# Kernel optimization log

Measured on AMD Instinct MI355X. Metric: run time of the kernel, lower is better.

The kernel has to match this reference:

```python
import jax, jax.numpy as jnp
import numpy as np
from jax import lax
jax.config.update("jax_enable_x64", True)

FNV_OFF = np.int64(-3750763034362895579)
FNV_PRIME = np.int64(4294967731)
I64_MAX = np.iinfo(np.int64).max
INF = np.float32(1e38)
CHUNK = 512  # cluster-chunk size for the cdist fallback


def _pack_key(b, c, vx, vy, vz):
    # five-word FNV-1a 64-bit hash with natural int64 wraparound
    h = jnp.full(b.shape, FNV_OFF, dtype=jnp.int64)
    for w in (b, c, vx, vy, vz):
        h = (h ^ w.astype(jnp.int64)) * FNV_PRIME
    return h


def _safe_norm(x):
    s = jnp.sum(x * x, axis=1)
    n = jnp.sqrt(jnp.where(s > 0, s, 1.0))
    return jnp.where(s > 0, n, 0.0)


def setup_inputs() -> dict:
    key = jax.random.key(0)
    k1, k2, k3, k4 = jax.random.split(key, 4)
    N = 65536
    grid = jax.random.randint(k1, (N, 3), 0, 400).astype(jnp.float32)
    batch_id = jnp.sort(jax.random.randint(k2, (N,), 0, 2).astype(jnp.int64))
    label = jax.random.randint(k3, (N,), 0, 8).astype(jnp.int64)
    pred_off = jax.random.normal(k4, (N, 3), dtype=jnp.float32)
    return {"pred_off": pred_off, "grid": grid, "label": label, "batch_id": batch_id,
            "base_grid": 16, "num_cls": 8, "num_batch": 2}


def _forward(pred_off, grid, label, batch_id, base_grid, num_cls, num_batch):
    N = grid.shape[0]
    grid_f = grid.astype(jnp.float32)
    vox = jnp.floor(grid_f / base_grid).astype(jnp.int64)  # [N,3]

    # voxel_grid: bucket by (batch, voxel) -> consecutive cluster ids via unique
    ckey = ((batch_id * 1024 + vox[:, 0]) * 1024 + vox[:, 1]) * 1024 + vox[:, 2]
    _, cluster = jnp.unique(ckey, return_inverse=True, size=N, fill_value=I64_MAX)
    cluster = cluster.reshape(-1)

    # cluster stats (segment scatter-reduce, num_segments = N upper bound)
    cnt = jax.ops.segment_sum(jnp.ones((N,), jnp.float32), cluster, num_segments=N)
    cl_center = jax.ops.segment_sum(grid_f, cluster, num_segments=N) / jnp.maximum(cnt, 1.0)[:, None]
    cl_batch = jax.ops.segment_min(batch_id, cluster, num_segments=N)
    cl_lbl_lo = jax.ops.segment_min(label, cluster, num_segments=N)
    cl_lbl_hi = jax.ops.segment_max(label, cluster, num_segments=N)
    cl_vox = jax.ops.segment_min(vox, cluster, num_segments=N)
    valid_cl = cnt > 0
    pure_cl = (cl_lbl_lo == cl_lbl_hi) & valid_cl
    pure_pt = pure_cl[cluster]

    # hash table of pure clusters, sorted by key (invalid -> sentinel, sorts last)
    pk_all = jnp.where(pure_cl, _pack_key(cl_batch, cl_lbl_lo, cl_vox[:, 0], cl_vox[:, 1], cl_vox[:, 2]), I64_MAX)
    order = jnp.argsort(pk_all)
    pk_sort = pk_all[order]
    pc_sort = cl_center[order]
    ok_sort = pure_cl[order]

    # per (batch,label) global centers
    key_bl = batch_id * num_cls + label
    nbl = num_batch * num_cls
    cnt_bl = jax.ops.segment_sum(jnp.ones((N,), jnp.float32), key_bl, num_segments=nbl)
    global_c = jax.ops.segment_sum(grid_f, key_bl, num_segments=nbl) / jnp.maximum(cnt_bl, 1.0)[:, None]
    step_sign = jnp.sign(global_c[key_bl] - cl_center[cluster]).astype(jnp.int64)  # [N,3]

    # +/-1 and +/-2 voxel hash lookup (steps 1 and K+1=2)
    def probe(step):
        cv = cl_vox[cluster] + step_sign * step
        ck = _pack_key(batch_id, label, cv[:, 0], cv[:, 1], cv[:, 2])
        idx = jnp.searchsorted(pk_sort, ck)
        idxc = jnp.minimum(idx, N - 1)
        hit = (idx < N) & ok_sort[idxc] & (pk_sort[idxc] == ck)
        return hit, pc_sort[idxc]

    hit1, t1 = probe(1)
    hit2, t2 = probe(2)
    hit_pt = hit1 | hit2
    tgt_c = jnp.where(hit1[:, None], t1, jnp.where(hit2[:, None], t2, grid_f))

    # fallback: nearest pure-cluster center with same (batch,label), chunked cdist+argmin
    miss = (~pure_pt) & (~hit_pt)
    code_y = key_bl
    code_x = jnp.where(pure_cl, cl_batch * num_cls + cl_lbl_lo, jnp.int64(-1))
    p2 = jnp.sum(grid_f * grid_f, axis=1)  # [N]

    def body(carry, i):
        best_d, best_c = carry
        c = lax.dynamic_slice_in_dim(cl_center, i * CHUNK, CHUNK)   # [S,3]
        cc = lax.dynamic_slice_in_dim(code_x, i * CHUNK, CHUNK)      # [S]
        d2 = p2[:, None] - 2.0 * (grid_f @ c.T) + jnp.sum(c * c, axis=1)[None, :]  # [N,S]
        d2 = jnp.where(cc[None, :] == code_y[:, None], d2, INF)
        j = jnp.argmin(d2, axis=1)
        dmin = jnp.take_along_axis(d2, j[:, None], axis=1)[:, 0]
        upd = dmin < best_d
        best_d = jnp.where(upd, dmin, best_d)
        best_c = jnp.where(upd[:, None], c[j], best_c)
        return (best_d, best_c), None

    nchunk = N // CHUNK
    (best_d, best_c), _ = lax.scan(body, (jnp.full((N,), INF, jnp.float32), grid_f), jnp.arange(nchunk))
    tgt_c = jnp.where((miss & (best_d < INF))[:, None], best_c, tgt_c)

    # loss: smooth-L1 on offsets below 99th-percentile magnitude + direction cosine loss
    tgt_off = tgt_c - grid_f
    mag = _safe_norm(tgt_off)
    thresh = jnp.quantile(mag, 0.99)
    m1 = mag <= thresh
    d = pred_off - tgt_off
    ad = jnp.abs(d)
    hub = jnp.where(ad < 1.0, 0.5 * d * d, ad - 0.5)
    n1 = jnp.sum(m1).astype(jnp.float32)
    loss_l1 = jnp.where(n1 > 0, jnp.sum(hub * m1[:, None]) / jnp.maximum(n1 * 3.0, 1.0), 0.0)

    md = (mag > 0) & m1
    eps = 1e-4
    pn = _safe_norm(pred_off)
    cos = jnp.sum(pred_off * tgt_off, axis=1) / jnp.maximum(pn * mag, eps)
    nmd = jnp.sum(md).astype(jnp.float32)
    loss_dir = jnp.where(nmd > 0, 1.0 - jnp.sum(cos * md) / jnp.maximum(nmd, 1.0), 0.0)
    return jnp.stack([loss_l1.astype(jnp.float32), loss_dir.astype(jnp.float32)])


def reference(pred_off, grid, label, batch_id, base_grid, num_cls, num_batch):
    return _forward(pred_off, grid, label, batch_id, base_grid, num_cls, num_batch)
```

## Files before the change

### kernel.cpp

```cpp
#include <hip/hip_runtime.h>
#include <climits>

#define VOXD 25
#define SLOT3 (VOXD*VOXD*VOXD)
#define SLOTS (2*SLOT3)
#define NCLS 8
#define NCODE 16
#define NBLK ((SLOTS + 255) / 256)
#define HB 2048
#define BPC 64
#define TILE 1024
#define CSTRIDE SLOT3

struct Scalars {
  double hub;
  double cosSum;
  int n1;
  int nmd;
  float thresh;
  int done;
  int done2;
};

__device__ __forceinline__ int voxslot(int b, int vx, int vy, int vz) {
  return ((b * VOXD + vx) * VOXD + vy) * VOXD + vz;
}

__device__ __forceinline__ int block_scan256(int v, int* ws) {
  int lane = threadIdx.x & 63, w = threadIdx.x >> 6;
  int s = v;
  #pragma unroll
  for (int off = 1; off < 64; off <<= 1) {
    int t = __shfl_up(s, off, 64);
    if (lane >= off) s += t;
  }
  if (lane == 63) ws[w] = s;
  __syncthreads();
  int add = 0;
  #pragma unroll
  for (int q = 0; q < 4; ++q) if (q < w) add += ws[q];
  __syncthreads();
  return s + add;
}

__global__ void k_scatter(const float* __restrict__ grid, const int* __restrict__ label,
                          const int* __restrict__ batch,
                          unsigned long long* vA, unsigned long long* vB, int* lmask,
                          int* blCnt, float* blSum, int n) {
  __shared__ int sCnt[NCODE];
  __shared__ float sSum[3 * NCODE];
  int tid = threadIdx.x;
  if (tid < NCODE) sCnt[tid] = 0;
  if (tid < 3 * NCODE) sSum[tid] = 0.f;
  __syncthreads();
  int i = blockIdx.x * blockDim.x + tid;
  if (i < n) {
    float gx = grid[3*i], gy = grid[3*i+1], gz = grid[3*i+2];
    int ix = (int)gx, iy = (int)gy, iz = (int)gz;
    int vx = (int)floorf(gx * (1.0f/16.0f));
    int vy = (int)floorf(gy * (1.0f/16.0f));
    int vz = (int)floorf(gz * (1.0f/16.0f));
    int b = batch[i], l = label[i];
    int s = voxslot(b, vx, vy, vz);
    atomicAdd(&vA[s], ((unsigned long long)(unsigned)ix << 32) | (unsigned)iy);
    atomicAdd(&vB[s], ((unsigned long long)(unsigned)iz << 24) | 1ULL);
    atomicOr(&lmask[s], 1 << l);
    int bl = b * NCLS + l;
    atomicAdd(&sCnt[bl], 1);
    atomicAdd(&sSum[3*bl], gx); atomicAdd(&sSum[3*bl+1], gy); atomicAdd(&sSum[3*bl+2], gz);
  }
  __syncthreads();
  if (tid < NCODE && sCnt[tid] != 0) atomicAdd(&blCnt[tid], sCnt[tid]);
  if (tid < 3 * NCODE && sSum[tid] != 0.f) atomicAdd(&blSum[tid], sSum[tid]);
}

__global__ void k_prep(const unsigned long long* vA, const unsigned long long* vB,
                       const int* lmask, float4* ctr, float4* pC, int* codeCnt) {
  __shared__ int lc[NCODE];
  __shared__ int lb[NCODE];
  int tid = threadIdx.x;
  if (tid < NCODE) lc[tid] = 0;
  __syncthreads();
  int s = blockIdx.x * 256 + tid;
  int code = -1, lpos = 0;
  float4 v = make_float4(0.f, 0.f, 0.f, __int_as_float(-2));
  if (s < SLOTS) {
    unsigned long long bq = vB[s];
    unsigned c = (unsigned)(bq & 0xFFFFFFULL);
    if (c > 0) {
      unsigned long long aq = vA[s];
      float fc = (float)c;
      float cx = __fdiv_rn((float)(unsigned)(aq >> 32), fc);
      float cy = __fdiv_rn((float)(unsigned)(aq & 0xFFFFFFFFULL), fc);
      float cz = __fdiv_rn((float)(unsigned)(bq >> 24), fc);
      int m = lmask[s];
      bool pure = (m & (m - 1)) == 0;
      int lbl = __ffs(m) - 1;
      v = make_float4(cx, cy, cz, __int_as_float(pure ? lbl : -1));
      if (pure) {
        code = (s / SLOT3) * NCLS + lbl;
        lpos = atomicAdd(&lc[code], 1);
      }
    }
    ctr[s] = v;
  }
  __syncthreads();
  if (tid < NCODE) lb[tid] = (lc[tid] > 0) ? atomicAdd(&codeCnt[tid], lc[tid]) : 0;
  __syncthreads();
  if (code >= 0) {
    int pos = code * CSTRIDE + lb[code] + lpos;
    pC[pos] = make_float4(v.x, v.y, v.z, __int_as_float(s));
  }
}

__global__ void k_targets(const float* __restrict__ grid, const int* __restrict__ label,
                          const int* __restrict__ batch,
                          const float4* __restrict__ ctr,
                          const int* __restrict__ blCnt, const float* __restrict__ blSum,
                          float* tgt, float* mag, int* ghist,
                          int* missPart, int* missCnt, int mstride, int n) {
  __shared__ int wCnt[4][NCODE];
  __shared__ int gBase[NCODE];
  __shared__ int h[HB];
  int tid = threadIdx.x, lane = tid & 63, w = tid >> 6;
  for (int t = tid; t < HB; t += 256) h[t] = 0;
  __syncthreads();
  int i = blockIdx.x * blockDim.x + tid;
  bool active = (i < n);
  bool miss = false;
  int mcode = -1;

  if (active) {
    float gx = grid[3*i], gy = grid[3*i+1], gz = grid[3*i+2];
    int vx = (int)floorf(gx * (1.0f/16.0f));
    int vy = (int)floorf(gy * (1.0f/16.0f));
    int vz = (int)floorf(gz * (1.0f/16.0f));
    int b = batch[i], l = label[i];
    int s = voxslot(b, vx, vy, vz);

    float4 own = ctr[s];
    bool purept = (__float_as_int(own.w) >= 0);

    int bl = b * NCLS + l;
    float fbc = (float)max(blCnt[bl], 1);
    float gcx = __fdiv_rn(blSum[3*bl],   fbc);
    float gcy = __fdiv_rn(blSum[3*bl+1], fbc);
    float gcz = __fdiv_rn(blSum[3*bl+2], fbc);

    float dx = __fsub_rn(gcx, own.x);
    float dy = __fsub_rn(gcy, own.y);
    float dz = __fsub_rn(gcz, own.z);
    int sgx = (dx > 0.f) ? 1 : ((dx < 0.f) ? -1 : 0);
    int sgy = (dy > 0.f) ? 1 : ((dy < 0.f) ? -1 : 0);
    int sgz = (dz > 0.f) ? 1 : ((dz < 0.f) ? -1 : 0);

    int ax1 = vx + sgx,     ay1 = vy + sgy,     az1 = vz + sgz;
    int ax2 = vx + 2 * sgx, ay2 = vy + 2 * sgy, az2 = vz + 2 * sgz;
    bool v1 = (unsigned)ax1 < (unsigned)VOXD && (unsigned)ay1 < (unsigned)VOXD &&
              (unsigned)az1 < (unsigned)VOXD;
    bool v2 = (unsigned)ax2 < (unsigned)VOXD && (unsigned)ay2 < (unsigned)VOXD &&
              (unsigned)az2 < (unsigned)VOXD;

    float4 q1 = make_float4(0.f, 0.f, 0.f, __int_as_float(-3));
    float4 q2 = q1;
    if (v1) q1 = ctr[voxslot(b, ax1, ay1, az1)];
    if (v2) q2 = ctr[voxslot(b, ax2, ay2, az2)];

    bool hit1 = v1 && (__float_as_int(q1.w) == l);
    bool hit2 = v2 && (__float_as_int(q2.w) == l);
    bool hit = hit1 || hit2;

    float tx = hit1 ? q1.x : (hit2 ? q2.x : gx);
    float ty = hit1 ? q1.y : (hit2 ? q2.y : gy);
    float tz = hit1 ? q1.z : (hit2 ? q2.z : gz);

    tgt[3*i] = tx; tgt[3*i+1] = ty; tgt[3*i+2] = tz;
    miss = (!purept && !hit);
    if (miss) {
      mcode = bl;
    } else {
      float tox = __fsub_rn(tx, gx), toy = __fsub_rn(ty, gy), toz = __fsub_rn(tz, gz);
      float ssq = __fadd_rn(__fadd_rn(__fmul_rn(tox,tox), __fmul_rn(toy,toy)),
                            __fmul_rn(toz,toz));
      float m = (ssq > 0.f) ? sqrtf(ssq) : 0.f;
      mag[i] = m;
      atomicAdd(&h[__float_as_uint(m) >> 21], 1);
    }
  }
  int myrank = 0;
  #pragma unroll
  for (int c = 0; c < NCODE; ++c) {
    unsigned long long mb = __ballot(mcode == c);
    if (lane == 0) wCnt[w][c] = __popcll(mb);
    if (mcode == c) myrank = __popcll(mb & ((1ULL << lane) - 1ULL));
  }
  __syncthreads();
  if (tid < NCODE) {
    int tot = wCnt[0][tid] + wCnt[1][tid] + wCnt[2][tid] + wCnt[3][tid];
    gBase[tid] = (tot > 0) ? atomicAdd(&missCnt[tid], tot) : 0;
  }
  __syncthreads();
  if (miss) {
    int base = gBase[mcode];
    for (int q = 0; q < 4; ++q) if (q < w) base += wCnt[q][mcode];
    missPart[mcode * mstride + base + myrank] = i;
  }
  for (int t = tid; t < HB; t += 256) {
    int c = h[t];
    if (c != 0) atomicAdd(&ghist[t], c);
  }
}

__global__ void __launch_bounds__(256) k_fallback(
    const float* __restrict__ grid,
    const float4* __restrict__ pC,
    const float4* __restrict__ ctr,
    const int* __restrict__ codeCnt,
    const int* __restrict__ missPart, const int* __restrict__ missCnt,
    float* tgt, float* mag, int* ghist, int mstride) {
  __shared__ float4 tile4[TILE];
  __shared__ int    stile[TILE];
  __shared__ unsigned long long bkeyw[4][64];
  __shared__ int h[HB];
  int tid = threadIdx.x, lane = tid & 63, w = tid >> 6;
  int c = blockIdx.x / BPC;
  int y = blockIdx.x % BPC;
  int mc = missCnt[c];
  if (y * 64 >= mc) return;
  int cc = codeCnt[c];
  int j0 = c * CSTRIDE;
  const int* mlist = missPart + c * mstride;

  for (int t = tid; t < HB; t += 256) h[t] = 0;
  __syncthreads();

  for (int t0 = y * 64; t0 < mc; t0 += BPC * 64) {
    int t = t0 + lane;
    bool valid = (t < mc);
    int idx = 0;
    float gx = 0.f, gy = 0.f, gz = 0.f, p2 = 0.f;
    if (valid) {
      idx = mlist[t];
      gx = grid[3*idx]; gy = grid[3*idx+1]; gz = grid[3*idx+2];
      p2 = __fadd_rn(__fadd_rn(__fmul_rn(gx,gx), __fmul_rn(gy,gy)),
                     __fmul_rn(gz,gz));
    }
    unsigned long long key = 0xFFFFFFFFFFFFFFFFULL;
    for (int tb = 0; tb < cc; tb += TILE) {
      int m = min(TILE, cc - tb);
      __syncthreads();
      for (int j = tid; j < m; j += 256) {
        float4 cl = pC[j0 + tb + j];
        float c2 = __fadd_rn(__fadd_rn(__fmul_rn(cl.x,cl.x), __fmul_rn(cl.y,cl.y)),
                             __fmul_rn(cl.z,cl.z));
        tile4[j] = make_float4(cl.x, cl.y, cl.z, c2);
        stile[j] = __float_as_int(cl.w);
      }
      __syncthreads();
      #pragma unroll 4
      for (int j = w; j < m; j += 4) {
        float4 cl = tile4[j];
        float dot = __fadd_rn(__fadd_rn(__fmul_rn(gx,cl.x), __fmul_rn(gy,cl.y)),
                              __fmul_rn(gz,cl.z));
        float d2 = __fadd_rn(__fsub_rn(p2, __fmul_rn(2.0f, dot)), cl.w);
        unsigned fb = __float_as_uint(d2);
        fb = (fb >> 31) ? ~fb : (fb | 0x80000000u);
        unsigned long long k2 = ((unsigned long long)fb << 32) | (unsigned)stile[j];
        if (k2 < key) key = k2;
      }
    }
    bkeyw[w][lane] = key;
    __syncthreads();
    if (w == 0 && valid) {
      unsigned long long k0 = bkeyw[0][lane];
      unsigned long long k1 = bkeyw[1][lane];
      unsigned long long k2_ = bkeyw[2][lane];
      unsigned long long k3 = bkeyw[3][lane];
      unsigned long long kk = k0 < k1 ? k0 : k1;
      unsigned long long kh = k2_ < k3 ? k2_ : k3;
      if (kh < kk) kk = kh;
      float mv = 0.f;
      if (cc > 0) {
        int slot = (int)(unsigned)(kk & 0xFFFFFFFFULL);
        float4 cl = ctr[slot];
        tgt[3*idx] = cl.x; tgt[3*idx+1] = cl.y; tgt[3*idx+2] = cl.z;
        float tox = __fsub_rn(cl.x, gx), toy = __fsub_rn(cl.y, gy),
              toz = __fsub_rn(cl.z, gz);
        float ssq = __fadd_rn(__fadd_rn(__fmul_rn(tox,tox), __fmul_rn(toy,toy)),
                              __fmul_rn(toz,toz));
        mv = (ssq > 0.f) ? sqrtf(ssq) : 0.f;
      }
      mag[idx] = mv;
      atomicAdd(&h[__float_as_uint(mv) >> 21], 1);
    }
    __syncthreads();
  }

  for (int t = tid; t < HB; t += 256) {
    int cv = h[t];
    if (cv != 0) atomicAdd(&ghist[t], cv);
  }
}

__global__ void __launch_bounds__(256) k_loss_sel(
    const float* __restrict__ pred, const float* __restrict__ grid,
    const float* __restrict__ tgt, const float* __restrict__ mag,
    const int* __restrict__ ghist, int* gh2A, int* gh2B,
    unsigned* dBits, double2* dHC, int* uCnt,
    Scalars* sc, float* out, int n, int nblocks, int r0, int r1, double tfrac) {
  __shared__ int h[HB];
  __shared__ int h2[HB];
  __shared__ int ws[4];
  __shared__ int s_misc[8];
  __shared__ double shH[256];
  __shared__ double shC[256];
  __shared__ int shN[256];
  __shared__ int shM[256];
  __shared__ int sLast;
  __shared__ float sTh;
  int tid = threadIdx.x, lane = tid & 63;

  int base8 = tid * 8;
  {
    int cbin[8];
    int s = 0;
    #pragma unroll
    for (int k = 0; k < 8; ++k) { cbin[k] = ghist[base8 + k]; s += cbin[k]; }
    int incl = block_scan256(s, ws);
    int lo = incl - s;
    if (r0 >= lo && r0 < lo + s) {
      int acc = lo;
      #pragma unroll
      for (int k = 0; k < 8; ++k) {
        if (r0 < acc + cbin[k]) { s_misc[0] = base8 + k; s_misc[1] = r0 - acc; break; }
        acc += cbin[k];
      }
    }
    if (r1 >= lo && r1 < lo + s) {
      int acc = lo;
      #pragma unroll
      for (int k = 0; k < 8; ++k) {
        if (r1 < acc + cbin[k]) { s_misc[2] = base8 + k; s_misc[3] = r1 - acc; break; }
        acc += cbin[k];
      }
    }
  }
  __syncthreads();
  int binA = s_misc[0], rA = s_misc[1], binB = s_misc[2], rB = s_misc[3];

  for (int t = tid; t < HB; t += 256) { h[t] = 0; h2[t] = 0; }
  __syncthreads();

  int i = blockIdx.x * 256 + tid;
  double hub = 0.0, cs = 0.0;
  int c1 = 0, cmd = 0;
  bool dfr = false;
  unsigned bits = 0;
  double dhub = 0.0, dcs = 0.0;
  if (i < n) {
    float m = mag[i];
    bits = __float_as_uint(m);
    int cb = (int)(bits >> 21);
    bool boundary = (cb == binA || cb == binB);
    if (boundary || cb < binA) {
      float tox = __fsub_rn(tgt[3*i],   grid[3*i]);
      float toy = __fsub_rn(tgt[3*i+1], grid[3*i+1]);
      float toz = __fsub_rn(tgt[3*i+2], grid[3*i+2]);
      float px = pred[3*i], py = pred[3*i+1], pz = pred[3*i+2];
      float d0 = __fsub_rn(px, tox), d1 = __fsub_rn(py, toy), d2 = __fsub_rn(pz, toz);
      float a0 = fabsf(d0), a1 = fabsf(d1), a2 = fabsf(d2);
      float h0 = (a0 < 1.f) ? __fmul_rn(__fmul_rn(0.5f, d0), d0) : __fsub_rn(a0, 0.5f);
      float h1 = (a1 < 1.f) ? __fmul_rn(__fmul_rn(0.5f, d1), d1) : __fsub_rn(a1, 0.5f);
      float h2v = (a2 < 1.f) ? __fmul_rn(__fmul_rn(0.5f, d2), d2) : __fsub_rn(a2, 0.5f);
      double hubv = (double)h0 + (double)h1 + (double)h2v;
      double csv = 0.0;
      if (m > 0.f) {
        float ps = __fadd_rn(__fadd_rn(__fmul_rn(px,px), __fmul_rn(py,py)), __fmul_rn(pz,pz));
        float pn = (ps > 0.f) ? sqrtf(ps) : 0.f;
        float dotp = __fadd_rn(__fadd_rn(__fmul_rn(px,tox), __fmul_rn(py,toy)),
                               __fmul_rn(pz,toz));
        float den = fmaxf(__fmul_rn(pn, m), 1e-4f);
        csv = (double)__fdiv_rn(dotp, den);
      }
      if (boundary) {
        dfr = true;
        dhub = hubv; dcs = csv;
        if (cb == binA) atomicAdd(&h[(bits >> 10) & 0x7FF], 1);
        if (cb == binB) atomicAdd(&h2[(bits >> 10) & 0x7FF], 1);
      } else {
        c1 = 1;
        hub = hubv;
        if (m > 0.f) { cmd = 1; cs = csv; }
      }
    }
  }
  {
    unsigned long long mb = __ballot(dfr);
    int mcp = __popcll(mb);
    int bs = 0;
    if (lane == 0 && mcp > 0) bs = atomicAdd(uCnt, mcp);
    bs = __shfl(bs, 0, 64);
    if (dfr) {
      int pos = bs + __popcll(mb & ((1ULL << lane) - 1ULL));
      dBits[pos] = bits;
      dHC[pos] = make_double2(dhub, dcs);
    }
  }
  __syncthreads();
  for (int t = tid; t < HB; t += 256) {
    int a = h[t];
    if (a != 0) atomicAdd(&gh2A[t], a);
    int b = h2[t];
    if (b != 0) atomicAdd(&gh2B[t], b);
  }

  shH[tid] = hub; shC[tid] = cs; shN[tid] = c1; shM[tid] = cmd;
  __syncthreads();
  for (int off = 128; off > 0; off >>= 1) {
    if (tid < off) {
      shH[tid] += shH[tid+off];
      shC[tid] += shC[tid+off];
      shN[tid] += shN[tid+off];
      shM[tid] += shM[tid+off];
    }
    __syncthreads();
  }
  if (tid == 0) {
    atomicAdd(&sc->hub, shH[0]);
    atomicAdd(&sc->cosSum, shC[0]);
    atomicAdd(&sc->n1, shN[0]);
    atomicAdd(&sc->nmd, shM[0]);
    __threadfence();
    int d = atomicAdd(&sc->done2, 1);
    sLast = (d == nblocks - 1) ? 1 : 0;
  }
  __syncthreads();
  if (!sLast) return;
  __threadfence();

  int U = atomicAdd(uCnt, 0);

  {
    int a8[8], sA = 0;
    #pragma unroll
    for (int k = 0; k < 8; ++k) { a8[k] = gh2A[base8 + k]; sA += a8[k]; }
    int inclA = block_scan256(sA, ws);
    int accA = inclA - sA;
    #pragma unroll
    for (int k = 0; k < 8; ++k) {
      if (rA >= accA && rA < accA + a8[k]) { s_misc[4] = base8 + k; s_misc[5] = rA - accA; }
      accA += a8[k];
    }
    int b8[8], sB = 0;
    #pragma unroll
    for (int k = 0; k < 8; ++k) { b8[k] = gh2B[base8 + k]; sB += b8[k]; }
    int inclB = block_scan256(sB, ws);
    int accB = inclB - sB;
    #pragma unroll
    for (int k = 0; k < 8; ++k) {
      if (rB >= accB && rB < accB + b8[k]) { s_misc[6] = base8 + k; s_misc[7] = rB - accB; }
      accB += b8[k];
    }
  }
  __syncthreads();
  int subA = s_misc[4], subRA = s_misc[5], subB = s_misc[6], subRB = s_misc[7];

  for (int t = tid; t < 1024; t += 256) { h[t] = 0; h2[t] = 0; }
  __syncthreads();
  {
    const uint4* b4 = (const uint4*)dBits;
    int nv = U >> 2;
    for (int v = tid; v < nv; v += 256) {
      uint4 u = b4[v];
      unsigned bb[4] = { u.x, u.y, u.z, u.w };
      #pragma unroll
      for (int k = 0; k < 4; ++k) {
        unsigned b0 = bb[k];
        int cb = (int)(b0 >> 21);
        if (cb == binA && (int)((b0 >> 10) & 0x7FF) == subA) atomicAdd(&h[b0 & 0x3FF], 1);
        if (cb == binB && (int)((b0 >> 10) & 0x7FF) == subB) atomicAdd(&h2[b0 & 0x3FF], 1);
      }
    }
    for (int t = (nv << 2) + tid; t < U; t += 256) {
      unsigned b0 = dBits[t];
      int cb = (int)(b0 >> 21);
      if (cb == binA && (int)((b0 >> 10) & 0x7FF) == subA) atomicAdd(&h[b0 & 0x3FF], 1);
      if (cb == binB && (int)((b0 >> 10) & 0x7FF) == subB) atomicAdd(&h2[b0 & 0x3FF], 1);
    }
  }
  __syncthreads();
  {
    int base4 = tid * 4;
    int la[4], sA = 0;
    #pragma unroll
    for (int k = 0; k < 4; ++k) { la[k] = h[base4 + k]; sA += la[k]; }
    int inclA = block_scan256(sA, ws);
    int accA = inclA - sA;
    #pragma unroll
    for (int k = 0; k < 4; ++k) {
      if (subRA >= accA && subRA < accA + la[k]) s_misc[0] = base4 + k;
      accA += la[k];
    }
    int lb4[4], sB = 0;
    #pragma unroll
    for (int k = 0; k < 4; ++k) { lb4[k] = h2[base4 + k]; sB += lb4[k]; }
    int inclB = block_scan256(sB, ws);
    int accB = inclB - sB;
    #pragma unroll
    for (int k = 0; k < 4; ++k) {
      if (subRB >= accB && subRB < accB + lb4[k]) s_misc[1] = base4 + k;
      accB += lb4[k];
    }
  }
  __syncthreads();
  if (tid == 0) {
    unsigned va = ((unsigned)binA << 21) | ((unsigned)subA << 10) | (unsigned)s_misc[0];
    unsigned vb = ((unsigned)binB << 21) | ((unsigned)subB << 10) | (unsigned)s_misc[1];
    double a = (double)__uint_as_float(va);
    double b = (double)__uint_as_float(vb);
    double th = (tfrac >= 0.5) ? (b - (b - a) * (1.0 - tfrac)) : (a + (b - a) * tfrac);
    sc->thresh = (float)th;
    sTh = (float)th;
  }
  __syncthreads();
  float th = sTh;

  double hub2 = 0.0, cs2 = 0.0;
  int c12 = 0, cmd2 = 0;
  for (int t = tid; t < U; t += 256) {
    unsigned v = dBits[t];
    float m = __uint_as_float(v);
    double2 hc = dHC[t];
    if (m <= th) {
      c12 += 1;
      hub2 += hc.x;
      if (m > 0.f) { cmd2 += 1; cs2 += hc.y; }
    }
  }
  shH[tid] = hub2; shC[tid] = cs2; shN[tid] = c12; shM[tid] = cmd2;
  __syncthreads();
  for (int off = 128; off > 0; off >>= 1) {
    if (tid < off) {
      shH[tid] += shH[tid+off];
      shC[tid] += shC[tid+off];
      shN[tid] += shN[tid+off];
      shM[tid] += shM[tid+off];
    }
    __syncthreads();
  }
  if (tid == 0) {
    double th_hub = atomicAdd(&sc->hub, 0.0) + shH[0];
    double th_cos = atomicAdd(&sc->cosSum, 0.0) + shC[0];
    int n1 = atomicAdd(&sc->n1, 0) + shN[0];
    int nmd = atomicAdd(&sc->nmd, 0) + shM[0];
    double l1 = (n1 > 0) ? th_hub / fmax((double)n1 * 3.0, 1.0) : 0.0;
    double ld = (nmd > 0) ? (1.0 - th_cos / fmax((double)nmd, 1.0)) : 0.0;
    out[0] = (float)l1;
    out[1] = (float)ld;
  }
}

extern "C" void kernel_launch(void* const* d_in, const int* in_sizes, int n_in,
                              void* d_out, int out_size, void* d_ws, size_t ws_size,
                              hipStream_t stream) {
  const float* pred  = (const float*)d_in[0];
  const float* grid  = (const float*)d_in[1];
  const int*   label = (const int*)d_in[2];
  const int*   batch = (const int*)d_in[3];
  int n = in_sizes[2];
  int mstride = n / 4;

  char* p = (char*)d_ws;
  auto take = [&](size_t bytes) -> char* {
    char* r = p;
    p += (bytes + 255) & ~(size_t)255;
    return r;
  };
  char* zbase = p;
  unsigned long long* vA = (unsigned long long*)take((size_t)SLOTS*8);
  unsigned long long* vB = (unsigned long long*)take((size_t)SLOTS*8);
  int*    lmask    = (int*)   take((size_t)SLOTS*4);
  int*    codeCnt  = (int*)   take(NCODE*4);
  int*    missCnt  = (int*)   take(NCODE*4);
  int*    blCnt    = (int*)   take(16*4);
  float*  blSum    = (float*) take(48*4);
  int*    ghist    = (int*)   take((size_t)HB*4);
  int*    gh2A     = (int*)   take((size_t)HB*4);
  int*    gh2B     = (int*)   take((size_t)HB*4);
  int*    uCnt     = (int*)   take(4);
  Scalars* sc      = (Scalars*)take(sizeof(Scalars));
  size_t zbytes = (size_t)(p - zbase);
  float4* ctr      = (float4*)take((size_t)SLOTS*16);
  float4* pC       = (float4*)take((size_t)NCODE*CSTRIDE*16);
  float*  tgt      = (float*) take((size_t)n*3*4);
  float*  mag      = (float*) take((size_t)n*4);
  int*    missPart = (int*)   take((size_t)NCODE*mstride*4);
  unsigned* dBits  = (unsigned*)take((size_t)n*4);
  double2*  dHC    = (double2*) take((size_t)n*16);

  int nb = (n + 255) / 256;
  int nfb = NCODE * BPC;

  double vi = 0.99 * (double)(n - 1);
  int r0 = (int)vi;
  int r1 = r0 + 1; if (r1 > n - 1) r1 = n - 1;
  double tfrac = vi - (double)r0;

  hipMemsetAsync(zbase, 0, zbytes, stream);
  k_scatter<<<nb, 256, 0, stream>>>(grid, label, batch, vA, vB, lmask,
                                    blCnt, blSum, n);
  k_prep<<<NBLK, 256, 0, stream>>>(vA, vB, lmask, ctr, pC, codeCnt);
  k_targets<<<nb, 256, 0, stream>>>(grid, label, batch, ctr, blCnt, blSum,
                                    tgt, mag, ghist, missPart, missCnt, mstride, n);
  k_fallback<<<nfb, 256, 0, stream>>>(grid, pC, ctr, codeCnt,
                                      missPart, missCnt, tgt, mag, ghist, mstride);
  k_loss_sel<<<nb, 256, 0, stream>>>(pred, grid, tgt, mag, ghist, gh2A, gh2B,
                                     dBits, dHC, uCnt, sc, (float*)d_out,
                                     n, nb, r0, r1, tfrac);
}
```

Before: 138.3 us.

## Fuse voxel prep into targets kernel and recompute centers from raw sums

Removes the separate k_prep kernel and the ctr center array. Pure-cluster compaction into pC now happens at the start of the targets kernel. Own and neighbor centers are recomputed on demand from the vA/vB atomic sums and lmask, and the fallback kernel does the same for its winning cluster. Part of the workspace zeroing moves from the memset into k_scatter, shrinking the memset to the accumulator arrays. This saves one launch and the ctr write/read traffic, at the cost of extra divisions and more scattered loads per point.

```diff
diff --git a/kernel.cpp b/kernel.cpp
--- a/kernel.cpp
+++ b/kernel.cpp
@@ -6,7 +6,6 @@
 #define SLOTS (2*SLOT3)
 #define NCLS 8
 #define NCODE 16
-#define NBLK ((SLOTS + 255) / 256)
 #define HB 2048
 #define BPC 64
 #define TILE 1024
@@ -46,10 +45,15 @@
 __global__ void k_scatter(const float* __restrict__ grid, const int* __restrict__ label,
                           const int* __restrict__ batch,
                           unsigned long long* vA, unsigned long long* vB, int* lmask,
-                          int* blCnt, float* blSum, int n) {
+                          int* blCnt, float* blSum, int* lateZero, int nzi, int n) {
   __shared__ int sCnt[NCODE];
   __shared__ float sSum[3 * NCODE];
   int tid = threadIdx.x;
+  {
+    int g = blockIdx.x * 256 + tid;
+    int stride = gridDim.x * 256;
+    for (int t = g; t < nzi; t += stride) lateZero[t] = 0;
+  }
   if (tid < NCODE) sCnt[tid] = 0;
   if (tid < 3 * NCODE) sSum[tid] = 0.f;
   __syncthreads();
@@ -74,63 +78,59 @@
   if (tid < 3 * NCODE && sSum[tid] != 0.f) atomicAdd(&blSum[tid], sSum[tid]);
 }
 
-__global__ void k_prep(const unsigned long long* vA, const unsigned long long* vB,
-                       const int* lmask, float4* ctr, float4* pC, int* codeCnt) {
-  __shared__ int lc[NCODE];
-  __shared__ int lb[NCODE];
-  int tid = threadIdx.x;
-  if (tid < NCODE) lc[tid] = 0;
-  __syncthreads();
-  int s = blockIdx.x * 256 + tid;
-  int code = -1, lpos = 0;
-  float4 v = make_float4(0.f, 0.f, 0.f, __int_as_float(-2));
-  if (s < SLOTS) {
-    unsigned long long bq = vB[s];
-    unsigned c = (unsigned)(bq & 0xFFFFFFULL);
-    if (c > 0) {
-      unsigned long long aq = vA[s];
-      float fc = (float)c;
-      float cx = __fdiv_rn((float)(unsigned)(aq >> 32), fc);
-      float cy = __fdiv_rn((float)(unsigned)(aq & 0xFFFFFFFFULL), fc);
-      float cz = __fdiv_rn((float)(unsigned)(bq >> 24), fc);
-      int m = lmask[s];
-      bool pure = (m & (m - 1)) == 0;
-      int lbl = __ffs(m) - 1;
-      v = make_float4(cx, cy, cz, __int_as_float(pure ? lbl : -1));
-      if (pure) {
-        code = (s / SLOT3) * NCLS + lbl;
-        lpos = atomicAdd(&lc[code], 1);
-      }
-    }
-    ctr[s] = v;
-  }
-  __syncthreads();
-  if (tid < NCODE) lb[tid] = (lc[tid] > 0) ? atomicAdd(&codeCnt[tid], lc[tid]) : 0;
-  __syncthreads();
-  if (code >= 0) {
-    int pos = code * CSTRIDE + lb[code] + lpos;
-    pC[pos] = make_float4(v.x, v.y, v.z, __int_as_float(s));
-  }
-}
-
-__global__ void k_targets(const float* __restrict__ grid, const int* __restrict__ label,
-                          const int* __restrict__ batch,
-                          const float4* __restrict__ ctr,
-                          const int* __restrict__ blCnt, const float* __restrict__ blSum,
-                          float* tgt, float* mag, int* ghist,
-                          int* missPart, int* missCnt, int mstride, int n) {
+__global__ void __launch_bounds__(256) k_targets_prep(
+    const float* __restrict__ grid, const int* __restrict__ label,
+    const int* __restrict__ batch,
+    const unsigned long long* __restrict__ vA, const unsigned long long* __restrict__ vB,
+    const int* __restrict__ lmask,
+    const int* __restrict__ blCnt, const float* __restrict__ blSum,
+    float4* pC, int* codeCnt,
+    float* tgt, float* mag, int* ghist,
+    int* missPart, int* missCnt, int mstride, int spb, int n) {
   __shared__ int wCnt[4][NCODE];
   __shared__ int gBase[NCODE];
   __shared__ int h[HB];
+  __shared__ int lc[NCODE];
+  __shared__ int lb[NCODE];
   int tid = threadIdx.x, lane = tid & 63, w = tid >> 6;
   for (int t = tid; t < HB; t += 256) h[t] = 0;
-  __syncthreads();
+  if (tid < NCODE) lc[tid] = 0;
+  __syncthreads();
+
+  int code = -1, lpos = 0;
+  int sSlot = blockIdx.x * spb + tid;
+  float pcx = 0.f, pcy = 0.f, pcz = 0.f;
+  if (tid < spb && sSlot < SLOTS) {
+    unsigned long long bq = vB[sSlot];
+    unsigned c = (unsigned)(bq & 0xFFFFFFULL);
+    if (c > 0) {
+      unsigned long long aq = vA[sSlot];
+      float fc = (float)c;
+      pcx = __fdiv_rn((float)(unsigned)(aq >> 32), fc);
+      pcy = __fdiv_rn((float)(unsigned)(aq & 0xFFFFFFFFULL), fc);
+      pcz = __fdiv_rn((float)(unsigned)(bq >> 24), fc);
+      int m = lmask[sSlot];
+      bool pure = (m & (m - 1)) == 0;
+      if (pure) {
+        int lbl = __ffs(m) - 1;
+        code = (sSlot / SLOT3) * NCLS + lbl;
+        lpos = atomicAdd(&lc[code], 1);
+      }
+    }
+  }
+  __syncthreads();
+  if (tid < NCODE) lb[tid] = (lc[tid] > 0) ? atomicAdd(&codeCnt[tid], lc[tid]) : 0;
+  __syncthreads();
+  if (code >= 0) {
+    int pos = code * CSTRIDE + lb[code] + lpos;
+    pC[pos] = make_float4(pcx, pcy, pcz, __int_as_float(sSlot));
+  }
+
   int i = blockIdx.x * blockDim.x + tid;
-  bool active = (i < n);
   bool miss = false;
   int mcode = -1;
 
-  if (active) {
+  if (i < n) {
     float gx = grid[3*i], gy = grid[3*i+1], gz = grid[3*i+2];
     int vx = (int)floorf(gx * (1.0f/16.0f));
     int vy = (int)floorf(gy * (1.0f/16.0f));
@@ -138,8 +138,15 @@
     int b = batch[i], l = label[i];
     int s = voxslot(b, vx, vy, vz);
 
-    float4 own = ctr[s];
-    bool purept = (__float_as_int(own.w) >= 0);
+    unsigned long long bqo = vB[s];
+    unsigned co = (unsigned)(bqo & 0xFFFFFFULL);
+    unsigned long long aqo = vA[s];
+    float fco = (float)co;
+    float ownx = __fdiv_rn((float)(unsigned)(aqo >> 32), fco);
+    float owny = __fdiv_rn((float)(unsigned)(aqo & 0xFFFFFFFFULL), fco);
+    float ownz = __fdiv_rn((float)(unsigned)(bqo >> 24), fco);
+    int mo = lmask[s];
+    bool purept = (mo & (mo - 1)) == 0;
 
     int bl = b * NCLS + l;
     float fbc = (float)max(blCnt[bl], 1);
@@ -147,9 +154,9 @@
     float gcy = __fdiv_rn(blSum[3*bl+1], fbc);
     float gcz = __fdiv_rn(blSum[3*bl+2], fbc);
 
-    float dx = __fsub_rn(gcx, own.x);
-    float dy = __fsub_rn(gcy, own.y);
-    float dz = __fsub_rn(gcz, own.z);
+    float dx = __fsub_rn(gcx, ownx);
+    float dy = __fsub_rn(gcy, owny);
+    float dz = __fsub_rn(gcz, ownz);
     int sgx = (dx > 0.f) ? 1 : ((dx < 0.f) ? -1 : 0);
     int sgy = (dy > 0.f) ? 1 : ((dy < 0.f) ? -1 : 0);
     int sgz = (dz > 0.f) ? 1 : ((dz < 0.f) ? -1 : 0);
@@ -161,21 +168,34 @@
     bool v2 = (unsigned)ax2 < (unsigned)VOXD && (unsigned)ay2 < (unsigned)VOXD &&
               (unsigned)az2 < (unsigned)VOXD;
 
-    float4 q1 = make_float4(0.f, 0.f, 0.f, __int_as_float(-3));
-    float4 q2 = q1;
-    if (v1) q1 = ctr[voxslot(b, ax1, ay1, az1)];
-    if (v2) q2 = ctr[voxslot(b, ax2, ay2, az2)];
-
-    bool hit1 = v1 && (__float_as_int(q1.w) == l);
-    bool hit2 = v2 && (__float_as_int(q2.w) == l);
-    bool hit = hit1 || hit2;
-
-    float tx = hit1 ? q1.x : (hit2 ? q2.x : gx);
-    float ty = hit1 ? q1.y : (hit2 ? q2.y : gy);
-    float tz = hit1 ? q1.z : (hit2 ? q2.z : gz);
+    int s1 = v1 ? voxslot(b, ax1, ay1, az1) : 0;
+    int s2 = v2 ? voxslot(b, ax2, ay2, az2) : 0;
+    bool hit1 = v1 && (lmask[s1] == (1 << l));
+    bool hit2 = v2 && (lmask[s2] == (1 << l));
+
+    float tx, ty, tz;
+    if (hit1) {
+      unsigned long long bq1 = vB[s1];
+      unsigned c1c = (unsigned)(bq1 & 0xFFFFFFULL);
+      unsigned long long aq1 = vA[s1];
+      float fc1 = (float)c1c;
+      tx = __fdiv_rn((float)(unsigned)(aq1 >> 32), fc1);
+      ty = __fdiv_rn((float)(unsigned)(aq1 & 0xFFFFFFFFULL), fc1);
+      tz = __fdiv_rn((float)(unsigned)(bq1 >> 24), fc1);
+    } else if (hit2) {
+      unsigned long long bq2 = vB[s2];
+      unsigned c2c = (unsigned)(bq2 & 0xFFFFFFULL);
+      unsigned long long aq2 = vA[s2];
+      float fc2 = (float)c2c;
+      tx = __fdiv_rn((float)(unsigned)(aq2 >> 32), fc2);
+      ty = __fdiv_rn((float)(unsigned)(aq2 & 0xFFFFFFFFULL), fc2);
+      tz = __fdiv_rn((float)(unsigned)(bq2 >> 24), fc2);
+    } else {
+      tx = gx; ty = gy; tz = gz;
+    }
 
     tgt[3*i] = tx; tgt[3*i+1] = ty; tgt[3*i+2] = tz;
-    miss = (!purept && !hit);
+    miss = (!purept && !hit1 && !hit2);
     if (miss) {
       mcode = bl;
     } else {
@@ -214,7 +234,7 @@
 __global__ void __launch_bounds__(256) k_fallback(
     const float* __restrict__ grid,
     const float4* __restrict__ pC,
-    const float4* __restrict__ ctr,
+    const unsigned long long* __restrict__ vA, const unsigned long long* __restrict__ vB,
     const int* __restrict__ codeCnt,
     const int* __restrict__ missPart, const int* __restrict__ missCnt,
     float* tgt, float* mag, int* ghist, int mstride) {
@@ -282,10 +302,16 @@
       float mv = 0.f;
       if (cc > 0) {
         int slot = (int)(unsigned)(kk & 0xFFFFFFFFULL);
-        float4 cl = ctr[slot];
-        tgt[3*idx] = cl.x; tgt[3*idx+1] = cl.y; tgt[3*idx+2] = cl.z;
-        float tox = __fsub_rn(cl.x, gx), toy = __fsub_rn(cl.y, gy),
-              toz = __fsub_rn(cl.z, gz);
+        unsigned long long bq = vB[slot];
+        unsigned cw = (unsigned)(bq & 0xFFFFFFULL);
+        unsigned long long aq = vA[slot];
+        float fc = (float)cw;
+        float cx_ = __fdiv_rn((float)(unsigned)(aq >> 32), fc);
+        float cy_ = __fdiv_rn((float)(unsigned)(aq & 0xFFFFFFFFULL), fc);
+        float cz_ = __fdiv_rn((float)(unsigned)(bq >> 24), fc);
+        tgt[3*idx] = cx_; tgt[3*idx+1] = cy_; tgt[3*idx+2] = cz_;
+        float tox = __fsub_rn(cx_, gx), toy = __fsub_rn(cy_, gy),
+              toz = __fsub_rn(cz_, gz);
         float ssq = __fadd_rn(__fadd_rn(__fmul_rn(tox,tox), __fmul_rn(toy,toy)),
                               __fmul_rn(toz,toz));
         mv = (ssq > 0.f) ? sqrtf(ssq) : 0.f;
@@ -576,21 +602,22 @@
     p += (bytes + 255) & ~(size_t)255;
     return r;
   };
-  char* zbase = p;
+  char* zbase1 = p;
   unsigned long long* vA = (unsigned long long*)take((size_t)SLOTS*8);
   unsigned long long* vB = (unsigned long long*)take((size_t)SLOTS*8);
   int*    lmask    = (int*)   take((size_t)SLOTS*4);
+  int*    blCnt    = (int*)   take(16*4);
+  float*  blSum    = (float*) take(48*4);
+  size_t zbytes1 = (size_t)(p - zbase1);
+  char* zbase2 = p;
   int*    codeCnt  = (int*)   take(NCODE*4);
   int*    missCnt  = (int*)   take(NCODE*4);
-  int*    blCnt    = (int*)   take(16*4);
-  float*  blSum    = (float*) take(48*4);
   int*    ghist    = (int*)   take((size_t)HB*4);
   int*    gh2A     = (int*)   take((size_t)HB*4);
   int*    gh2B     = (int*)   take((size_t)HB*4);
   int*    uCnt     = (int*)   take(4);
   Scalars* sc      = (Scalars*)take(sizeof(Scalars));
-  size_t zbytes = (size_t)(p - zbase);
-  float4* ctr      = (float4*)take((size_t)SLOTS*16);
+  size_t zbytes2 = (size_t)(p - zbase2);
   float4* pC       = (float4*)take((size_t)NCODE*CSTRIDE*16);
   float*  tgt      = (float*) take((size_t)n*3*4);
   float*  mag      = (float*) take((size_t)n*4);
@@ -599,20 +626,24 @@
   double2*  dHC    = (double2*) take((size_t)n*16);
 
   int nb = (n + 255) / 256;
+  int grid2 = nb > ((SLOTS + 255) / 256) ? nb : ((SLOTS + 255) / 256);
+  int spb = (SLOTS + grid2 - 1) / grid2;
   int nfb = NCODE * BPC;
+  int nzi = (int)(zbytes2 / 4);
 
   double vi = 0.99 * (double)(n - 1);
   int r0 = (int)vi;
   int r1 = r0 + 1; if (r1 > n - 1) r1 = n - 1;
   double tfrac = vi - (double)r0;
 
-  hipMemsetAsync(zbase, 0, zbytes, stream);
+  hipMemsetAsync(zbase1, 0, zbytes1, stream);
   k_scatter<<<nb, 256, 0, stream>>>(grid, label, batch, vA, vB, lmask,
-                                    blCnt, blSum, n);
-  k_prep<<<NBLK, 256, 0, stream>>>(vA, vB, lmask, ctr, pC, codeCnt);
-  k_targets<<<nb, 256, 0, stream>>>(grid, label, batch, ctr, blCnt, blSum,
-                                    tgt, mag, ghist, missPart, missCnt, mstride, n);
-  k_fallback<<<nfb, 256, 0, stream>>>(grid, pC, ctr, codeCnt,
+                                    blCnt, blSum, (int*)zbase2, nzi, n);
+  k_targets_prep<<<grid2, 256, 0, stream>>>(grid, label, batch, vA, vB, lmask,
+                                            blCnt, blSum, pC, codeCnt,
+                                            tgt, mag, ghist, missPart, missCnt,
+                                            mstride, spb, n);
+  k_fallback<<<nfb, 256, 0, stream>>>(grid, pC, vA, vB, codeCnt,
                                       missPart, missCnt, tgt, mag, ghist, mstride);
   k_loss_sel<<<nb, 256, 0, stream>>>(pred, grid, tgt, mag, ghist, gh2A, gh2B,
                                      dBits, dHC, uCnt, sc, (float*)d_out,
```

New measurement: 138.3 us. About the same (+0.0%).
